# Kernel optimization log

Hardware: AMD Instinct MI355X
Metric: run time of the kernel (lower is better)

The kernel has to match this reference:

```python
import jax, jax.numpy as jnp
import numpy as np


def gcn_conv(x, row, col, W, b, n_nodes):
    """PyG GCNConv: x' = D^-1/2 (A+I) D^-1/2 (x W) + b, with self-loops in row/col."""
    xw = x @ W  # [N, out]
    deg = jax.ops.segment_sum(jnp.ones_like(col, dtype=xw.dtype), col, num_segments=n_nodes)
    d_inv_sqrt = jnp.where(deg > 0, jax.lax.rsqrt(deg), 0.0)
    norm = d_inv_sqrt[row] * d_inv_sqrt[col]  # [E+N]
    msgs = norm[:, None] * xw[row]            # gather + scale
    out = jax.ops.segment_sum(msgs, col, num_segments=n_nodes)  # scatter-add to dst
    return out + b


def setup_inputs() -> dict:
    key = jax.random.key(0)
    ks = jax.random.split(key, 8)
    N, E = 100000, 1600000
    d_in, d_h, d_out = 128, 128, 64
    x = jax.random.normal(ks[0], (N, d_in), dtype=jnp.float32)
    edge_index = jax.random.randint(ks[1], (2, E), 0, N, dtype=jnp.int32)
    s = 1.0 / np.sqrt(d_in)
    W1 = jax.random.uniform(ks[2], (d_in, d_h), jnp.float32, -s, s)
    b1 = jnp.zeros((d_h,), jnp.float32)
    sh = 1.0 / np.sqrt(d_h)
    W2 = jax.random.uniform(ks[3], (d_h, d_h), jnp.float32, -sh, sh)
    b2 = jnp.zeros((d_h,), jnp.float32)
    W3 = jax.random.uniform(ks[4], (d_h, d_out), jnp.float32, -sh, sh)
    b3 = jnp.zeros((d_out,), jnp.float32)
    return {"x": x, "edge_index": edge_index, "W1": W1, "b1": b1,
            "W2": W2, "b2": b2, "W3": W3, "b3": b3}


def reference(x, edge_index, W1, b1, W2, b2, W3, b3):
    n_nodes = x.shape[0]
    loops = jnp.arange(n_nodes, dtype=edge_index.dtype)
    row = jnp.concatenate([edge_index[0], loops])  # src (with self-loops)
    col = jnp.concatenate([edge_index[1], loops])  # dst (with self-loops)
    # dropout p=0.0 / eval mode -> identity, omitted
    h = jax.nn.relu(gcn_conv(x, row, col, W1, b1, n_nodes))
    h = jax.nn.relu(gcn_conv(h, row, col, W2, b2, n_nodes))
    out = gcn_conv(h, row, col, W3, b3, n_nodes)
    return out
```

## Files before the change

### kernel.cpp

```cpp
#include <hip/hip_runtime.h>
#include <hip/hip_fp16.h>

typedef _Float16 half8 __attribute__((ext_vector_type(8)));
typedef float floatx4 __attribute__((ext_vector_type(4)));
typedef unsigned long long u64;

#define NCH 128
#define TILE 2048
#define CSLOT 48
#define MAXCH2 800
#define PLCAP 14336
#define OVFCAP 65536
#define AGG_GRID 2048

__global__ __launch_bounds__(256) void part_k(const int* __restrict__ row,
                                              const int* __restrict__ col, int E,
                                              int chunk, int NB,
                                              u64* __restrict__ stg_p,
                                              int* __restrict__ cnts,
                                              int* __restrict__ chunkTot,
                                              u64* __restrict__ ovf,
                                              int* __restrict__ ovfcnt,
                                              const float* __restrict__ W1,
                                              const float* __restrict__ W2,
                                              const float* __restrict__ W3,
                                              __half* __restrict__ Wt1,
                                              __half* __restrict__ Wt2,
                                              __half* __restrict__ Wt3) {
    __shared__ u64 bkt[NCH][CSLOT];
    __shared__ int lcnt[NCH];
    __shared__ int lpref[NCH + 1];
    int tid = threadIdx.x;
    int b = blockIdx.x;

    int idx = b * 256 + tid;
    if (idx < 16384) {
        int k = idx >> 7, nn = idx & 127;
        Wt1[nn * 128 + k] = __float2half(W1[idx]);
    } else if (idx < 32768) {
        int j = idx - 16384;
        int k = j >> 7, nn = j & 127;
        Wt2[nn * 128 + k] = __float2half(W2[j]);
    } else if (idx < 40960) {
        int j = idx - 32768;
        int k = j >> 6, nn = j & 63;
        Wt3[nn * 128 + k] = __float2half(W3[j]);
    }

    for (int i = tid; i < NCH; i += 256) lcnt[i] = 0;
    __syncthreads();

    int i0 = b * TILE + tid * 8;
    int sv[8], dv[8];
    int nv = 0;
    if (i0 + 7 < E && (E & 3) == 0) {
        int4 r0 = *(const int4*)(row + i0);
        int4 r1 = *(const int4*)(row + i0 + 4);
        int4 c0 = *(const int4*)(col + i0);
        int4 c1 = *(const int4*)(col + i0 + 4);
        sv[0] = r0.x; sv[1] = r0.y; sv[2] = r0.z; sv[3] = r0.w;
        sv[4] = r1.x; sv[5] = r1.y; sv[6] = r1.z; sv[7] = r1.w;
        dv[0] = c0.x; dv[1] = c0.y; dv[2] = c0.z; dv[3] = c0.w;
        dv[4] = c1.x; dv[5] = c1.y; dv[6] = c1.z; dv[7] = c1.w;
        nv = 8;
    } else {
#pragma unroll
        for (int j = 0; j < 8; j++) {
            if (i0 + j < E) { sv[nv] = row[i0 + j]; dv[nv] = col[i0 + j]; nv++; }
        }
    }
#pragma unroll 8
    for (int j = 0; j < nv; j++) {
        int d = dv[j], s = sv[j];
        int c = d / chunk;
        int r = atomicAdd(&lcnt[c], 1);
        u64 pair = ((u64)(unsigned)d << 32) | (unsigned)s;
        if (r < CSLOT) {
            bkt[c][r] = pair;
        } else {
            int o = atomicAdd(ovfcnt, 1);
            if (o < OVFCAP) ovf[o] = pair;
        }
    }
    __syncthreads();
    if (tid < NCH) {
        int cc = min(lcnt[tid], CSLOT);
        lcnt[tid] = cc;
        cnts[(size_t)tid * NB + b] = cc;
        atomicAdd(&chunkTot[tid * 16], cc);
    }
    __syncthreads();
    if (tid == 0) {
        int a = 0;
#pragma unroll
        for (int c = 0; c < NCH; c++) {
            lpref[c] = a;
            a += lcnt[c];
        }
        lpref[NCH] = a;
    }
    __syncthreads();
    int total = lpref[NCH];
    for (int f = tid; f < total; f += 256) {
        int lo = 0, hi = NCH;
        while (hi - lo > 1) {
            int mid = (lo + hi) >> 1;
            if (lpref[mid] <= f) lo = mid; else hi = mid;
        }
        int slot = f - lpref[lo];
        stg_p[((size_t)lo * NB + b) * CSLOT + slot] = bkt[lo][slot];
    }
}

__global__ __launch_bounds__(512) void csr_build_k(const u64* __restrict__ stg_p,
                                                   const int* __restrict__ cnts,
                                                   const int* __restrict__ chunkTot,
                                                   int NB, int N, int chunk,
                                                   const u64* __restrict__ ovf,
                                                   const int* __restrict__ ovfcnt,
                                                   float* __restrict__ dinv,
                                                   int* __restrict__ cptr,
                                                   int* __restrict__ meta) {
    __shared__ int hist[MAXCH2];
    __shared__ int cur[MAXCH2];
    __shared__ int sc[512];
    __shared__ u64 pl[PLCAP];
    __shared__ int plcnt;
    int c = blockIdx.x, tid = threadIdx.x;
    int dlo = c * chunk;
    int dhi = min(N, dlo + chunk);
    int csz = dhi - dlo;
    if (csz <= 0) return;
    if (tid == 0) plcnt = 0;
    for (int i = tid; i < csz; i += 512) hist[i] = 1;

    int part = 0;
    for (int i = tid; i < c; i += 512) part += chunkTot[i * 16];
    int oc = min(*ovfcnt, OVFCAP);
    for (int i = tid; i < oc; i += 512) {
        int d = (int)(ovf[i] >> 32);
        if (d < dlo) part++;
    }
    sc[tid] = part;
    __syncthreads();
    for (int o = 256; o > 0; o >>= 1) {
        if (tid < o) sc[tid] += sc[tid + o];
        __syncthreads();
    }
    int cbase = dlo + sc[0];
    __syncthreads();

    for (int b0 = tid >> 4; b0 < NB; b0 += 32) {
        int cnt = cnts[(size_t)c * NB + b0];
        size_t base = ((size_t)c * NB + b0) * CSLOT;
        for (int slot = tid & 15; slot < cnt; slot += 16) {
            u64 v = stg_p[base + slot];
            atomicAdd(&hist[(int)(v >> 32) - dlo], 1);
            int p = atomicAdd(&plcnt, 1);
            if (p < PLCAP) pl[p] = v;
        }
    }
    for (int i = tid; i < oc; i += 512) {
        int d = (int)(ovf[i] >> 32);
        if (d >= dlo && d < dhi) atomicAdd(&hist[d - dlo], 1);
    }
    __syncthreads();

    int i0 = tid * 2;
    int v0 = (i0 < csz) ? hist[i0] : 0;
    int v1 = (i0 + 1 < csz) ? hist[i0 + 1] : 0;
    int s = v0 + v1;
    sc[tid] = s;
    __syncthreads();
    for (int o = 1; o < 512; o <<= 1) {
        int tmp = 0;
        if (tid >= o) tmp = sc[tid - o];
        __syncthreads();
        sc[tid] += tmp;
        __syncthreads();
    }
    int off = cbase + sc[tid] - s;
    if (i0 < csz) {
        cur[i0] = off;
        cptr[dlo + i0] = off;
        dinv[dlo + i0] = rsqrtf((float)v0);
        off += v0;
        if (i0 + 1 < csz) {
            cur[i0 + 1] = off;
            cptr[dlo + i0 + 1] = off;
            dinv[dlo + i0 + 1] = rsqrtf((float)v1);
        }
    }
    if (dhi == N && tid == 511) cptr[N] = cbase + sc[511];
    __syncthreads();

    int pc = plcnt;
    if (pc <= PLCAP) {
        for (int i = tid; i < pc; i += 512) {
            u64 v = pl[i];
            int p = atomicAdd(&cur[(int)(v >> 32) - dlo], 1);
            meta[p] = (int)(v & 0xffffffffULL);
        }
    } else {
        for (int b0 = tid >> 4; b0 < NB; b0 += 32) {
            int cnt = cnts[(size_t)c * NB + b0];
            size_t base = ((size_t)c * NB + b0) * CSLOT;
            for (int slot = tid & 15; slot < cnt; slot += 16) {
                u64 v = stg_p[base + slot];
                int p = atomicAdd(&cur[(int)(v >> 32) - dlo], 1);
                meta[p] = (int)(v & 0xffffffffULL);
            }
        }
    }
    for (int i = tid; i < csz; i += 512) {
        int p = atomicAdd(&cur[i], 1);
        meta[p] = dlo + i;
    }
    for (int i = tid; i < oc; i += 512) {
        u64 v = ovf[i];
        int d = (int)(v >> 32);
        if (d >= dlo && d < dhi) {
            int p = atomicAdd(&cur[d - dlo], 1);
            meta[p] = (int)(v & 0xffffffffULL);
        }
    }
}

template <typename AT, int DOUT>
__global__ __launch_bounds__(256) void gemm_mfma(const AT* __restrict__ A,
                                                 const __half* __restrict__ Wt,
                                                 const float* __restrict__ dinv,
                                                 __half* __restrict__ C, int n) {
    constexpr int CT = DOUT / 16;
    constexpr int WP = 136;
    __shared__ _Float16 ldsW[DOUT * WP];
    int tid = threadIdx.x;
    int lane = tid & 63;
    int wid = tid >> 6;
    for (int i = tid; i < DOUT * 16; i += 256) {
        int nrow = i >> 4;
        int kc = (i & 15) * 8;
        *(half8*)(&ldsW[nrow * WP + kc]) =
            *(const half8*)((const _Float16*)Wt + nrow * 128 + kc);
    }
    __syncthreads();
    int rwb = blockIdx.x * 128 + wid * 32;
    int m = lane & 15;
    int quad = lane >> 4;
    floatx4 acc[2][CT];
#pragma unroll
    for (int t = 0; t < 2; t++)
#pragma unroll
        for (int c = 0; c < CT; c++) acc[t][c] = (floatx4){0.f, 0.f, 0.f, 0.f};

#pragma unroll
    for (int kq = 0; kq < 4; kq++) {
        int k0 = kq * 32 + quad * 8;
        half8 afr[2];
#pragma unroll
        for (int t = 0; t < 2; t++) {
            int r = rwb + t * 16 + m;
            r = r < n ? r : n - 1;
            const AT* ap = A + (size_t)r * 128 + k0;
            if constexpr (sizeof(AT) == 2) {
                afr[t] = *(const half8*)ap;
            } else {
                float4 f0 = *(const float4*)ap;
                float4 f1 = *(const float4*)(ap + 4);
                half8 h;
                h[0] = (_Float16)f0.x; h[1] = (_Float16)f0.y;
                h[2] = (_Float16)f0.z; h[3] = (_Float16)f0.w;
                h[4] = (_Float16)f1.x; h[5] = (_Float16)f1.y;
                h[6] = (_Float16)f1.z; h[7] = (_Float16)f1.w;
                afr[t] = h;
            }
        }
#pragma unroll
        for (int c = 0; c < CT; c++) {
            half8 bfr = *(const half8*)(&ldsW[(c * 16 + m) * WP + k0]);
#pragma unroll
            for (int t = 0; t < 2; t++)
                acc[t][c] =
                    __builtin_amdgcn_mfma_f32_16x16x32_f16(afr[t], bfr, acc[t][c], 0, 0, 0);
        }
    }
#pragma unroll
    for (int t = 0; t < 2; t++) {
#pragma unroll
        for (int reg = 0; reg < 4; reg++) {
            int r = rwb + t * 16 + quad * 4 + reg;
            if (r < n) {
                float dv = dinv[r];
#pragma unroll
                for (int c = 0; c < CT; c++)
                    C[(size_t)r * DOUT + c * 16 + m] = __float2half(acc[t][c][reg] * dv);
            }
        }
    }
    if (blockIdx.x == 0 && tid < DOUT / 8) {
        half8 z = (half8){0, 0, 0, 0, 0, 0, 0, 0};
        *(half8*)((_Float16*)C + (size_t)n * DOUT + tid * 8) = z;
    }
}

template <int D, bool RELU, typename OT>
__global__ __launch_bounds__(256) void aggregate_k(const __half* __restrict__ xw,
                                                   const int* __restrict__ ptr,
                                                   const int* __restrict__ meta,
                                                   const float* __restrict__ bias,
                                                   const float* __restrict__ dinv,
                                                   OT* __restrict__ out, int n) {
    constexpr int GS = D / 8;
    constexpr int EPW = 64 / GS;
    constexpr int UNR = 4;
    __shared__ int smeta[4][64];
    int lane = threadIdx.x & 63;
    int wid = threadIdx.x >> 6;
    int sub = lane / GS;
    int cg = lane % GS;
    const _Float16* xp = (const _Float16*)xw + cg * 8;

    for (int node = blockIdx.x * 4 + wid; node < n; node += gridDim.x * 4) {
        int e0 = ptr[node], e1 = ptr[node + 1];
        float dv = dinv[node];
        float acc[8];
#pragma unroll
        for (int i = 0; i < 8; i++) acc[i] = 0.f;

        for (int base = e0; base < e1; base += 64) {
            int cnt = min(e1 - base, 64);
            if (lane < cnt) smeta[wid][lane] = meta[base + lane];
            for (int j = 0; j < cnt; j += UNR * EPW) {
                int sreg[UNR];
#pragma unroll
                for (int u = 0; u < UNR; u++) {
                    int e = j + u * EPW + sub;
                    int t = smeta[wid][e];
                    sreg[u] = (e < cnt) ? t : n;
                }
                half8 vreg[UNR];
#pragma unroll
                for (int u = 0; u < UNR; u++)
                    vreg[u] = *(const half8*)(xp + (size_t)sreg[u] * D);
#pragma unroll
                for (int u = 0; u < UNR; u++)
#pragma unroll
                    for (int i = 0; i < 8; i++)
                        acc[i] += (float)vreg[u][i];
            }
        }
#pragma unroll
        for (int off = GS; off < 64; off <<= 1) {
#pragma unroll
            for (int i = 0; i < 8; i++) acc[i] += __shfl_xor(acc[i], off, 64);
        }
        if (lane < GS) {
            float4 bb0 = *(const float4*)(bias + cg * 8);
            float4 bb1 = *(const float4*)(bias + cg * 8 + 4);
            float r[8];
            r[0] = acc[0] * dv + bb0.x; r[1] = acc[1] * dv + bb0.y;
            r[2] = acc[2] * dv + bb0.z; r[3] = acc[3] * dv + bb0.w;
            r[4] = acc[4] * dv + bb1.x; r[5] = acc[5] * dv + bb1.y;
            r[6] = acc[6] * dv + bb1.z; r[7] = acc[7] * dv + bb1.w;
            if (RELU) {
#pragma unroll
                for (int i = 0; i < 8; i++) r[i] = fmaxf(r[i], 0.f);
            }
            if constexpr (sizeof(OT) == 2) {
                half8 h;
#pragma unroll
                for (int i = 0; i < 8; i++) h[i] = (_Float16)r[i];
                *(half8*)((_Float16*)out + (size_t)node * D + cg * 8) = h;
            } else {
                float* op = (float*)out + (size_t)node * D + cg * 8;
                *(float4*)op = make_float4(r[0], r[1], r[2], r[3]);
                *(float4*)(op + 4) = make_float4(r[4], r[5], r[6], r[7]);
            }
        }
    }
}

extern "C" void kernel_launch(void* const* d_in, const int* in_sizes, int n_in,
                              void* d_out, int out_size, void* d_ws, size_t ws_size,
                              hipStream_t stream) {
    const float* x = (const float*)d_in[0];
    const int* ei = (const int*)d_in[1];
    const float* W1 = (const float*)d_in[2];
    const float* b1 = (const float*)d_in[3];
    const float* W2 = (const float*)d_in[4];
    const float* b2 = (const float*)d_in[5];
    const float* W3 = (const float*)d_in[6];
    const float* b3 = (const float*)d_in[7];
    float* out = (float*)d_out;
    int N = in_sizes[0] / 128;
    int E = in_sizes[1] / 2;
    const int* row = ei;
    const int* col = ei + E;
    int T = E + N;

    char* w = (char*)d_ws;
    size_t off = 0;
    auto alloc = [&](size_t bytes) -> void* {
        void* p = w + off;
        off = (off + bytes + 511) & ~(size_t)511;
        return p;
    };
    __half* bufH = (__half*)alloc((size_t)(N + 1) * 128 * 2);
    __half* bufA = (__half*)alloc((size_t)N * 128 * 2);
    __half* Wt1 = (__half*)alloc(16384 * 2);
    __half* Wt2 = (__half*)alloc(16384 * 2);
    __half* Wt3 = (__half*)alloc(8192 * 2);
    float* dinv = (float*)alloc((size_t)N * 4);
    int* cptr = (int*)alloc((size_t)(N + 1) * 4);
    int* meta = (int*)alloc((size_t)T * 4);
    int* ctblock = (int*)alloc(128 * 64 + 64);
    u64* ovf = (u64*)alloc((size_t)OVFCAP * 8);
    int NB = (E + TILE - 1) / TILE;
    int* cnts = (int*)alloc((size_t)NCH * NB * 4);
    int chunk = (N + NCH - 1) / NCH;

    int* chunkTot = ctblock;
    int* ovfcnt = ctblock + 2048;

    u64* stg_p = (u64*)d_ws;

    hipMemsetAsync(ctblock, 0, 128 * 64 + 64, stream);
    part_k<<<NB, 256, 0, stream>>>(row, col, E, chunk, NB, stg_p, cnts, chunkTot,
                                   ovf, ovfcnt, W1, W2, W3, Wt1, Wt2, Wt3);
    csr_build_k<<<NCH, 512, 0, stream>>>(stg_p, cnts, chunkTot, NB, N, chunk, ovf,
                                         ovfcnt, dinv, cptr, meta);

    int gb = (N + 127) / 128;
    gemm_mfma<float, 128><<<gb, 256, 0, stream>>>(x, Wt1, dinv, bufH, N);
    aggregate_k<128, true, __half><<<AGG_GRID, 256, 0, stream>>>(bufH, cptr, meta, b1, dinv, bufA, N);
    gemm_mfma<__half, 128><<<gb, 256, 0, stream>>>(bufA, Wt2, dinv, bufH, N);
    aggregate_k<128, true, __half><<<AGG_GRID, 256, 0, stream>>>(bufH, cptr, meta, b2, dinv, bufA, N);
    gemm_mfma<__half, 64><<<gb, 256, 0, stream>>>(bufA, Wt3, dinv, bufH, N);
    aggregate_k<64, false, float><<<AGG_GRID, 256, 0, stream>>>(bufH, cptr, meta, b3, dinv, out, N);
}
```

Measured before the change: 366.1 us.

## Double CSR build chunks, use per-block overflow buckets, and deepen aggregation unroll

Raises the destination chunk count from 128 to 256, so the CSR build runs on twice as many blocks, and shrinks per-chunk shared slots to match. The global overflow counter and the chunkTot atomics are replaced by per-block overflow buffers and counts, and chunk offsets are now summed from the cnts array, which removes the memset and global atomics. The aggregation kernel unrolls 8 when there are 4 edges per wave pass and hoists the bias loads out of the node loop. In exchange, every build block now reads a prefix of cnts and scans all per-block overflow lists whenever any overflow exists.

```diff
diff --git a/kernel.cpp b/kernel.cpp
--- a/kernel.cpp
+++ b/kernel.cpp
@@ -5,12 +5,12 @@
 typedef float floatx4 __attribute__((ext_vector_type(4)));
 typedef unsigned long long u64;
 
-#define NCH 128
+#define NCH 256
 #define TILE 2048
-#define CSLOT 48
-#define MAXCH2 800
-#define PLCAP 14336
-#define OVFCAP 65536
+#define CSLOT 28
+#define MAXCH2 400
+#define PLCAP 7168
+#define OVFB 512
 #define AGG_GRID 2048
 
 __global__ __launch_bounds__(256) void part_k(const int* __restrict__ row,
@@ -18,9 +18,8 @@
                                               int chunk, int NB,
                                               u64* __restrict__ stg_p,
                                               int* __restrict__ cnts,
-                                              int* __restrict__ chunkTot,
                                               u64* __restrict__ ovf,
-                                              int* __restrict__ ovfcnt,
+                                              int* __restrict__ ovfcnt_arr,
                                               const float* __restrict__ W1,
                                               const float* __restrict__ W2,
                                               const float* __restrict__ W3,
@@ -30,6 +29,7 @@
     __shared__ u64 bkt[NCH][CSLOT];
     __shared__ int lcnt[NCH];
     __shared__ int lpref[NCH + 1];
+    __shared__ int lovf;
     int tid = threadIdx.x;
     int b = blockIdx.x;
 
@@ -48,6 +48,7 @@
     }
 
     for (int i = tid; i < NCH; i += 256) lcnt[i] = 0;
+    if (tid == 0) lovf = 0;
     __syncthreads();
 
     int i0 = b * TILE + tid * 8;
@@ -78,17 +79,17 @@
         if (r < CSLOT) {
             bkt[c][r] = pair;
         } else {
-            int o = atomicAdd(ovfcnt, 1);
-            if (o < OVFCAP) ovf[o] = pair;
-        }
-    }
-    __syncthreads();
-    if (tid < NCH) {
+            int o = atomicAdd(&lovf, 1);
+            if (o < OVFB) ovf[(size_t)b * OVFB + o] = pair;
+        }
+    }
+    __syncthreads();
+    {
         int cc = min(lcnt[tid], CSLOT);
         lcnt[tid] = cc;
         cnts[(size_t)tid * NB + b] = cc;
-        atomicAdd(&chunkTot[tid * 16], cc);
-    }
+    }
+    if (tid == 0) ovfcnt_arr[b] = min(lovf, OVFB);
     __syncthreads();
     if (tid == 0) {
         int a = 0;
@@ -114,10 +115,9 @@
 
 __global__ __launch_bounds__(512) void csr_build_k(const u64* __restrict__ stg_p,
                                                    const int* __restrict__ cnts,
-                                                   const int* __restrict__ chunkTot,
+                                                   const int* __restrict__ ovfcnt_arr,
                                                    int NB, int N, int chunk,
                                                    const u64* __restrict__ ovf,
-                                                   const int* __restrict__ ovfcnt,
                                                    float* __restrict__ dinv,
                                                    int* __restrict__ cptr,
                                                    int* __restrict__ meta) {
@@ -134,12 +134,26 @@
     if (tid == 0) plcnt = 0;
     for (int i = tid; i < csz; i += 512) hist[i] = 1;
 
+    int myo = 0;
+    for (int i = tid; i < NB; i += 512) myo += ovfcnt_arr[i];
+    sc[tid] = myo;
+    __syncthreads();
+    for (int o = 256; o > 0; o >>= 1) {
+        if (tid < o) sc[tid] += sc[tid + o];
+        __syncthreads();
+    }
+    int totOvf = sc[0];
+    __syncthreads();
+
     int part = 0;
-    for (int i = tid; i < c; i += 512) part += chunkTot[i * 16];
-    int oc = min(*ovfcnt, OVFCAP);
-    for (int i = tid; i < oc; i += 512) {
-        int d = (int)(ovf[i] >> 32);
-        if (d < dlo) part++;
+    int lim = c * NB;
+    for (int i = tid; i < lim; i += 512) part += cnts[i];
+    if (totOvf) {
+        for (int b = 0; b < NB; b++) {
+            int oc = ovfcnt_arr[b];
+            for (int j = tid; j < oc; j += 512)
+                if ((int)(ovf[(size_t)b * OVFB + j] >> 32) < dlo) part++;
+        }
     }
     sc[tid] = part;
     __syncthreads();
@@ -160,9 +174,14 @@
             if (p < PLCAP) pl[p] = v;
         }
     }
-    for (int i = tid; i < oc; i += 512) {
-        int d = (int)(ovf[i] >> 32);
-        if (d >= dlo && d < dhi) atomicAdd(&hist[d - dlo], 1);
+    if (totOvf) {
+        for (int b = 0; b < NB; b++) {
+            int oc = ovfcnt_arr[b];
+            for (int j = tid; j < oc; j += 512) {
+                int d = (int)(ovf[(size_t)b * OVFB + j] >> 32);
+                if (d >= dlo && d < dhi) atomicAdd(&hist[d - dlo], 1);
+            }
+        }
     }
     __syncthreads();
 
@@ -216,12 +235,17 @@
         int p = atomicAdd(&cur[i], 1);
         meta[p] = dlo + i;
     }
-    for (int i = tid; i < oc; i += 512) {
-        u64 v = ovf[i];
-        int d = (int)(v >> 32);
-        if (d >= dlo && d < dhi) {
-            int p = atomicAdd(&cur[d - dlo], 1);
-            meta[p] = (int)(v & 0xffffffffULL);
+    if (totOvf) {
+        for (int b = 0; b < NB; b++) {
+            int oc = ovfcnt_arr[b];
+            for (int j = tid; j < oc; j += 512) {
+                u64 v = ovf[(size_t)b * OVFB + j];
+                int d = (int)(v >> 32);
+                if (d >= dlo && d < dhi) {
+                    int p = atomicAdd(&cur[d - dlo], 1);
+                    meta[p] = (int)(v & 0xffffffffULL);
+                }
+            }
         }
     }
 }
@@ -312,13 +336,15 @@
                                                    OT* __restrict__ out, int n) {
     constexpr int GS = D / 8;
     constexpr int EPW = 64 / GS;
-    constexpr int UNR = 4;
+    constexpr int UNR = (EPW == 4) ? 8 : 4;
     __shared__ int smeta[4][64];
     int lane = threadIdx.x & 63;
     int wid = threadIdx.x >> 6;
     int sub = lane / GS;
     int cg = lane % GS;
     const _Float16* xp = (const _Float16*)xw + cg * 8;
+    float4 bb0 = *(const float4*)(bias + cg * 8);
+    float4 bb1 = *(const float4*)(bias + cg * 8 + 4);
 
     for (int node = blockIdx.x * 4 + wid; node < n; node += gridDim.x * 4) {
         int e0 = ptr[node], e1 = ptr[node + 1];
@@ -335,8 +361,9 @@
 #pragma unroll
                 for (int u = 0; u < UNR; u++) {
                     int e = j + u * EPW + sub;
+                    e = (e < 64) ? e : 0;
                     int t = smeta[wid][e];
-                    sreg[u] = (e < cnt) ? t : n;
+                    sreg[u] = (j + u * EPW + sub < cnt) ? t : n;
                 }
                 half8 vreg[UNR];
 #pragma unroll
@@ -355,8 +382,6 @@
             for (int i = 0; i < 8; i++) acc[i] += __shfl_xor(acc[i], off, 64);
         }
         if (lane < GS) {
-            float4 bb0 = *(const float4*)(bias + cg * 8);
-            float4 bb1 = *(const float4*)(bias + cg * 8 + 4);
             float r[8];
             r[0] = acc[0] * dv + bb0.x; r[1] = acc[1] * dv + bb0.y;
             r[2] = acc[2] * dv + bb0.z; r[3] = acc[3] * dv + bb0.w;
@@ -413,22 +438,18 @@
     float* dinv = (float*)alloc((size_t)N * 4);
     int* cptr = (int*)alloc((size_t)(N + 1) * 4);
     int* meta = (int*)alloc((size_t)T * 4);
-    int* ctblock = (int*)alloc(128 * 64 + 64);
-    u64* ovf = (u64*)alloc((size_t)OVFCAP * 8);
     int NB = (E + TILE - 1) / TILE;
     int* cnts = (int*)alloc((size_t)NCH * NB * 4);
+    int* ovfcnt_arr = (int*)alloc((size_t)NB * 4);
+    u64* ovf = (u64*)alloc((size_t)NB * OVFB * 8);
     int chunk = (N + NCH - 1) / NCH;
 
-    int* chunkTot = ctblock;
-    int* ovfcnt = ctblock + 2048;
-
     u64* stg_p = (u64*)d_ws;
 
-    hipMemsetAsync(ctblock, 0, 128 * 64 + 64, stream);
-    part_k<<<NB, 256, 0, stream>>>(row, col, E, chunk, NB, stg_p, cnts, chunkTot,
-                                   ovf, ovfcnt, W1, W2, W3, Wt1, Wt2, Wt3);
-    csr_build_k<<<NCH, 512, 0, stream>>>(stg_p, cnts, chunkTot, NB, N, chunk, ovf,
-                                         ovfcnt, dinv, cptr, meta);
+    part_k<<<NB, 256, 0, stream>>>(row, col, E, chunk, NB, stg_p, cnts, ovf,
+                                   ovfcnt_arr, W1, W2, W3, Wt1, Wt2, Wt3);
+    csr_build_k<<<NCH, 512, 0, stream>>>(stg_p, cnts, ovfcnt_arr, NB, N, chunk, ovf,
+                                         dinv, cptr, meta);
 
     int gb = (N + 127) / 128;
     gemm_mfma<float, 128><<<gb, 256, 0, stream>>>(x, Wt1, dinv, bufH, N);
```

After: 427.5 us. 1.17x slower.
